# Performance work log

Measured on AMD Instinct MI355X. Metric: run time of the kernel, lower is better.

The kernel has to match this reference:

```python
import jax, jax.numpy as jnp
import numpy as np

D_HEAD = 64


def precompute_rope(d_head, max_seq_len):
    theta = 10000.0 ** (-jnp.arange(0, d_head, 2, dtype=jnp.float32) / d_head)
    positions = jnp.arange(max_seq_len, dtype=jnp.float32)
    angles = jnp.outer(positions, theta)  # [T, d_head/2]
    cos = jnp.repeat(jnp.cos(angles), 2, axis=-1)  # [T, d_head]
    sin = jnp.repeat(jnp.sin(angles), 2, axis=-1)
    return cos, sin


def apply_rope(x, cos, sin):
    # x: [B, H, T, d_head]; cos/sin: [T, d_head] (already sliced to T)
    x_even = x[..., 0::2]
    x_odd = x[..., 1::2]
    x2 = jnp.stack([-x_odd, x_even], axis=-1).reshape(x.shape)  # rotate-half interleaved
    return x * cos + x2 * sin


def setup_inputs() -> dict:
    key = jax.random.key(0)
    k1, k2, k3 = jax.random.split(key, 3)
    B, T, C = 4, 2048, 1024
    x = jax.random.normal(k1, (B, T, C), dtype=jnp.float32)
    mask = jnp.tril(jnp.ones((T, T), dtype=jnp.int32))[None, None]  # causal [1,1,T,T]
    Wqkv = jax.random.normal(k2, (3 * C, C), dtype=jnp.float32) * (1.0 / np.sqrt(C))
    Wout = jax.random.normal(k3, (C, C), dtype=jnp.float32) * (1.0 / np.sqrt(C))
    return {"x": x, "mask": mask, "Wqkv": Wqkv, "Wout": Wout}


def reference(x, mask, Wqkv, Wout):
    B, T, C = x.shape
    n_heads = 16
    d_head = C // n_heads
    cos, sin = precompute_rope(d_head, T)

    qkv = (x @ Wqkv.T).reshape(B, T, 3, n_heads, d_head)
    q, k, v = qkv[:, :, 0], qkv[:, :, 1], qkv[:, :, 2]
    q = jnp.transpose(q, (0, 2, 1, 3))  # [B, H, T, d]
    k = jnp.transpose(k, (0, 2, 1, 3))
    v = jnp.transpose(v, (0, 2, 1, 3))

    q = apply_rope(q, cos, sin)
    k = apply_rope(k, cos, sin)

    attn = jnp.einsum('bhqd,bhkd->bhqk', q, k) / jnp.sqrt(jnp.float32(d_head))
    attn = jnp.where(mask[:, :, :T, :T] == 0, -jnp.inf, attn)
    attn = jax.nn.softmax(attn, axis=-1)

    out = jnp.einsum('bhqk,bhkd->bhqd', attn, v)
    out = jnp.transpose(out, (0, 2, 1, 3)).reshape(B, T, C)
    return out @ Wout.T
```

## Files before the change

kernel.cpp:

```cpp
#include <hip/hip_runtime.h>

typedef unsigned short u16;
typedef unsigned int   u32;
typedef __bf16 bf16;
typedef bf16  bf16x8 __attribute__((ext_vector_type(8)));
typedef u16   u16x8  __attribute__((ext_vector_type(8)));
typedef u32   u32x4  __attribute__((ext_vector_type(4)));
typedef float f32x4  __attribute__((ext_vector_type(4)));
typedef float f32x16 __attribute__((ext_vector_type(16)));

__device__ __forceinline__ u16 f2bf(float f) {
  u32 u = __builtin_bit_cast(u32, f);
  u32 r = u + 0x7fffu + ((u >> 16) & 1u);
  return (u16)(r >> 16);
}

__device__ __forceinline__ u32 cvtpk(float lo, float hi) {
  u32 r;
  asm("v_cvt_pk_bf16_f32 %0, %1, %2" : "=v"(r) : "v"(lo), "v"(hi));
  return r;
}

__device__ __forceinline__ bf16x8 ldb8(const u16* p) {
  return __builtin_bit_cast(bf16x8, *reinterpret_cast<const u16x8*>(p));
}

__device__ __forceinline__ f32x4 mfma16(bf16x8 a, bf16x8 b, f32x4 c) {
  return __builtin_amdgcn_mfma_f32_16x16x32_bf16(a, b, c, 0, 0, 0);
}

__device__ __forceinline__ f32x16 mfma32(bf16x8 a, bf16x8 b, f32x16 c) {
  return __builtin_amdgcn_mfma_f32_32x32x16_bf16(a, b, c, 0, 0, 0);
}

__device__ __forceinline__ void gl_lds16(const void* g, void* l) {
  __builtin_amdgcn_global_load_lds(
      (const __attribute__((address_space(1))) void*)g,
      (__attribute__((address_space(3))) void*)l, 16, 0, 0);
}

__device__ __forceinline__ void stage128x64(const u16* gbase, u16* lds, int tid) {
#pragma unroll
  for (int rd = 0; rd < 4; rd++) {
    int o = rd * 4096 + tid * 16;
    int row = o >> 7, colb = o & 127;
    gl_lds16((const char*)gbase + (size_t)row * 2048 + colb, (char*)lds + o);
  }
}

__device__ __forceinline__ size_t qk_frag_addr(int bh, int t, int d) {
  return (size_t)bh * 131072 + (size_t)(t >> 5) * 2048 +
         (size_t)((d >> 4) * 512 + ((d >> 3) & 1) * 256 + (t & 31) * 8 + (d & 7));
}
__device__ __forceinline__ size_t v_frag_addr(int bh, int t, int d) {
  return (size_t)bh * 131072 + (size_t)(t >> 5) * 2048 +
         (size_t)((d >> 5) * 1024 + ((t >> 4) & 1) * 512 +
                  (((t >> 3) & 1) * 32 + (d & 31)) * 8 + (t & 7));
}

__global__ void cvt_bf16(const float* __restrict__ in, u16* __restrict__ out, int n4) {
  int stride = gridDim.x * blockDim.x;
  for (int i = blockIdx.x * blockDim.x + threadIdx.x; i < n4; i += stride) {
    float4 f = reinterpret_cast<const float4*>(in)[i];
    ushort4 o;
    o.x = f2bf(f.x); o.y = f2bf(f.y); o.z = f2bf(f.z); o.w = f2bf(f.w);
    reinterpret_cast<ushort4*>(out)[i] = o;
  }
}

__global__ void rope_tab(float* __restrict__ ct, float* __restrict__ st) {
  int idx = blockIdx.x * 256 + threadIdx.x;
  int t = idx >> 5, i = idx & 31;
  float theta = exp2f(-(float)i * 0.4152410118609203f);
  float ang = (float)t * theta;
  ct[idx] = cosf(ang);
  st[idx] = sinf(ang);
}

__global__ __launch_bounds__(256) void gemm_qkv(
    const u16* __restrict__ xb, const u16* __restrict__ wb,
    u16* __restrict__ qfb, u16* __restrict__ kfb, u16* __restrict__ vfb,
    const float* __restrict__ cost, const float* __restrict__ sint) {
  __shared__ u16 As[128 * 64];
  __shared__ u16 Bs[128 * 64];
  int tid = threadIdx.x, lane = tid & 63, w = tid >> 6;
  int wm = w >> 1, wn = w & 1;
  int lr = lane & 15, lk = lane >> 4;
  int m0 = blockIdx.y * 128, n0 = blockIdx.x * 128;

  f32x4 acc[4][4] = {};

  for (int k0 = 0; k0 < 1024; k0 += 64) {
    stage128x64(xb + (size_t)m0 * 1024 + k0, As, tid);
    stage128x64(wb + (size_t)n0 * 1024 + k0, Bs, tid);
    asm volatile("s_waitcnt vmcnt(0)" ::: "memory");
    __syncthreads();
#pragma unroll
    for (int kk = 0; kk < 2; kk++) {
      bf16x8 af[4], bfr[4];
#pragma unroll
      for (int mt = 0; mt < 4; mt++) af[mt]  = ldb8(&As[(64 * wm + 16 * mt + lr) * 64 + lk * 8 + 32 * kk]);
#pragma unroll
      for (int nt = 0; nt < 4; nt++) bfr[nt] = ldb8(&Bs[(64 * wn + 16 * nt + lr) * 64 + lk * 8 + 32 * kk]);
#pragma unroll
      for (int mt = 0; mt < 4; mt++)
#pragma unroll
        for (int nt = 0; nt < 4; nt++)
          acc[mt][nt] = mfma16(af[mt], bfr[nt], acc[mt][nt]);
    }
    __syncthreads();
  }

  const float CQ = 0.18033688011112042f;
#pragma unroll
  for (int nt = 0; nt < 4; nt++) {
    int col = n0 + 64 * wn + 16 * nt + lr;
    int sec = col >> 10;
    int cc = col & 1023;
    int h = cc >> 6, d = cc & 63;
    if (sec < 2) {
      u16* buf = (sec == 0) ? qfb : kfb;
      float scale = (sec == 0) ? CQ : 1.0f;
#pragma unroll
      for (int mt = 0; mt < 4; mt++) {
        int Mb = m0 + 64 * wm + 16 * mt + lk * 4;
#pragma unroll
        for (int r = 0; r < 4; r++) {
          int M = Mb + r;
          int b = M >> 11, t = M & 2047;
          float val = acc[mt][nt][r];
          float par = __shfl_xor(val, 1);
          float c_ = cost[t * 32 + (d >> 1)];
          float s_ = sint[t * 32 + (d >> 1)];
          float res = (d & 1) ? (val * c_ + par * s_) : (val * c_ - par * s_);
          buf[qk_frag_addr(b * 16 + h, t, d)] = f2bf(res * scale);
        }
      }
    } else {
#pragma unroll
      for (int mt = 0; mt < 4; mt++) {
        int Mb = m0 + 64 * wm + 16 * mt + lk * 4;
        int b = Mb >> 11, t = Mb & 2047;
        ushort4 pk;
        pk.x = f2bf(acc[mt][nt][0]); pk.y = f2bf(acc[mt][nt][1]);
        pk.z = f2bf(acc[mt][nt][2]); pk.w = f2bf(acc[mt][nt][3]);
        *reinterpret_cast<ushort4*>(&vfb[v_frag_addr(b * 16 + h, t, d)]) = pk;
      }
    }
  }
}


__device__ __forceinline__ void attn_step(
    const u16* __restrict__ kfb, const u16* __restrict__ vfb,
    const bf16x8* qf, int kt, int qt, int qrow,
    int lane, int hi,
    f32x16& o0, f32x16& o1, float& m_, float& l_) {
  const u16* ktb = kfb + (size_t)kt * 2048;
  const u16* vtb = vfb + (size_t)kt * 2048;
  bf16x8 vf00 = ldb8(vtb + lane * 8);
  bf16x8 vf01 = ldb8(vtb + 512 + lane * 8);
  bf16x8 vf10 = ldb8(vtb + 1024 + lane * 8);
  bf16x8 vf11 = ldb8(vtb + 1536 + lane * 8);

  f32x16 sT = {};
#pragma unroll
  for (int s = 0; s < 4; s++) {
    bf16x8 kf = ldb8(ktb + s * 512 + lane * 8);
    sT = mfma32(kf, qf[s], sT);
  }
  if (kt == qt) {
    int k0 = kt * 32;
#pragma unroll
    for (int r = 0; r < 16; r++) {
      int kvg = k0 + (r & 3) + 8 * (r >> 2) + 4 * hi;
      if (kvg > qrow) sT[r] = -3.0e38f;
    }
  }
  float a0 = fmaxf(fmaxf(sT[0], sT[1]),  fmaxf(sT[2], sT[3]));
  float a1 = fmaxf(fmaxf(sT[4], sT[5]),  fmaxf(sT[6], sT[7]));
  float a2 = fmaxf(fmaxf(sT[8], sT[9]),  fmaxf(sT[10], sT[11]));
  float a3 = fmaxf(fmaxf(sT[12], sT[13]), fmaxf(sT[14], sT[15]));
  float pm = fmaxf(fmaxf(a0, a1), fmaxf(a2, a3));
  pm = fmaxf(pm, __shfl_xor(pm, 32));

  if (__any(pm > m_ + 8.0f)) {
    float mn = fmaxf(m_, pm);
    float corr = exp2f(m_ - mn);
    l_ *= corr;
    o0 *= corr; o1 *= corr;
    m_ = mn;
  }

  float p[16];
#pragma unroll
  for (int r = 0; r < 16; r++) p[r] = exp2f(sT[r] - m_);
  float r0 = (p[0] + p[1]) + (p[2] + p[3]);
  float r1 = (p[4] + p[5]) + (p[6] + p[7]);
  float r2 = (p[8] + p[9]) + (p[10] + p[11]);
  float r3 = (p[12] + p[13]) + (p[14] + p[15]);
  float rs = (r0 + r1) + (r2 + r3);
  rs += __shfl_xor(rs, 32);
  l_ += rs;

  u32 c0 = cvtpk(p[0], p[1]),   c1 = cvtpk(p[2], p[3]);
  u32 c2 = cvtpk(p[4], p[5]),   c3 = cvtpk(p[6], p[7]);
  u32 c4 = cvtpk(p[8], p[9]),   c5 = cvtpk(p[10], p[11]);
  u32 c6 = cvtpk(p[12], p[13]), c7 = cvtpk(p[14], p[15]);
  u32 x0 = __shfl_xor((int)c0, 32), x1 = __shfl_xor((int)c1, 32);
  u32 x2 = __shfl_xor((int)c2, 32), x3 = __shfl_xor((int)c3, 32);
  u32 x4 = __shfl_xor((int)c4, 32), x5 = __shfl_xor((int)c5, 32);
  u32 x6 = __shfl_xor((int)c6, 32), x7 = __shfl_xor((int)c7, 32);
  u32x4 w0 = { hi ? x2 : c0, hi ? x3 : c1, hi ? c2 : x0, hi ? c3 : x1 };
  u32x4 w1 = { hi ? x6 : c4, hi ? x7 : c5, hi ? c6 : x4, hi ? c7 : x5 };
  bf16x8 pf0 = __builtin_bit_cast(bf16x8, w0);
  bf16x8 pf1 = __builtin_bit_cast(bf16x8, w1);

  o0 = mfma32(vf00, pf0, o0);
  o0 = mfma32(vf01, pf1, o0);
  o1 = mfma32(vf10, pf0, o1);
  o1 = mfma32(vf11, pf1, o1);
}

__device__ __forceinline__ void stash_state(
    float* o_l, float* ml, int lane,
    const f32x16& o0, const f32x16& o1, float m_, float l_) {
#pragma unroll
  for (int r = 0; r < 16; r++) {
    o_l[r * 64 + lane]        = o0[r];
    o_l[(16 + r) * 64 + lane] = o1[r];
  }
  ml[lane]      = m_;
  ml[64 + lane] = l_;
}

__device__ __forceinline__ void merge_state(
    const float* o_l, const float* ml, int lane,
    f32x16& o0, f32x16& o1, float& m_, float& l_) {
  float me = ml[lane], le = ml[64 + lane];
  float mn = fmaxf(m_, me);
  float sc = exp2f(m_ - mn), se = exp2f(me - mn);
  l_ = l_ * sc + le * se;
#pragma unroll
  for (int r = 0; r < 16; r++) {
    o0[r] = o0[r] * sc + o_l[r * 64 + lane] * se;
    o1[r] = o1[r] * sc + o_l[(16 + r) * 64 + lane] * se;
  }
  m_ = mn;
}

__device__ __forceinline__ void attn_half(
    const u16* __restrict__ qfb, const u16* __restrict__ kfb,
    const u16* __restrict__ vfb, u16* __restrict__ og,
    float* o_lds, float* ml_lds,
    int qt, int kt0, int w, int lane, int l31, int hi,
    size_t outbase) {
  int qrow = qt * 32 + l31;
  bf16x8 qf[4];
#pragma unroll
  for (int s = 0; s < 4; s++)
    qf[s] = ldb8(qfb + (size_t)qt * 2048 + s * 512 + lane * 8);

  f32x16 o0 = {}, o1 = {};
  float m_ = -3.0e38f, l_ = 0.f;

#pragma unroll 1
  for (int kt = kt0; kt <= qt; kt += 4)
    attn_step(kfb, vfb, qf, kt, qt, qrow, lane, hi, o0, o1, m_, l_);

  if (w >= 2) stash_state(o_lds + (w - 2) * 2048, ml_lds + (w - 2) * 128, lane, o0, o1, m_, l_);
  __syncthreads();
  if (w < 2)  merge_state(o_lds + w * 2048, ml_lds + w * 128, lane, o0, o1, m_, l_);
  __syncthreads();
  if (w == 1) stash_state(o_lds, ml_lds, lane, o0, o1, m_, l_);
  __syncthreads();
  if (w == 0) {
    merge_state(o_lds, ml_lds, lane, o0, o1, m_, l_);
    float inv = 1.0f / l_;
    size_t base = outbase + (size_t)qrow * 1024;
#pragma unroll
    for (int db = 0; db < 2; db++) {
      f32x16 oo = db ? o1 : o0;
#pragma unroll
      for (int r = 0; r < 16; r += 2) {
        int d = db * 32 + (r & 3) + 8 * (r >> 2) + 4 * hi;
        u32 pk_ = cvtpk(oo[r] * inv, oo[r + 1] * inv);
        *reinterpret_cast<u32*>(&og[base + d]) = pk_;
      }
    }
  }
  __syncthreads();
}

__global__ __launch_bounds__(256, 4) void attn_fwd(
    const u16* __restrict__ qg, const u16* __restrict__ kg,
    const u16* __restrict__ vg, u16* __restrict__ og) {
  __shared__ float o_lds[2 * 32 * 64];
  __shared__ float ml_lds[2 * 2 * 64];
  int tid = threadIdx.x, lane = tid & 63, w = tid >> 6;
  int l31 = lane & 31, hi = lane >> 5;
  int blk = blockIdx.x;
  int bh = blk & 63, i = blk >> 6;
  const u16* qfb = qg + (size_t)bh * 131072;
  const u16* kfb = kg + (size_t)bh * 131072;
  const u16* vfb = vg + (size_t)bh * 131072;
  int hh = bh & 15, b = bh >> 4;
  size_t outbase = (size_t)b * 2048 * 1024 + hh * 64;

  attn_half(qfb, kfb, vfb, og, o_lds, ml_lds, i, w, w, lane, l31, hi, outbase);
  attn_half(qfb, kfb, vfb, og, o_lds, ml_lds, 63 - i, (w - i - 1) & 3, w, lane, l31, hi, outbase);
}

__global__ __launch_bounds__(256) void gemm_out(
    const u16* __restrict__ ab, const u16* __restrict__ wb, float* __restrict__ out) {
  __shared__ u16 As[128 * 64];
  __shared__ u16 Bs[128 * 64];
  int tid = threadIdx.x, lane = tid & 63, w = tid >> 6;
  int wm = w >> 1, wn = w & 1;
  int lr = lane & 15, lk = lane >> 4;
  int m0 = blockIdx.y * 128, n0 = blockIdx.x * 128;

  f32x4 acc[4][4] = {};

  for (int k0 = 0; k0 < 1024; k0 += 64) {
    stage128x64(ab + (size_t)m0 * 1024 + k0, As, tid);
    stage128x64(wb + (size_t)n0 * 1024 + k0, Bs, tid);
    asm volatile("s_waitcnt vmcnt(0)" ::: "memory");
    __syncthreads();
#pragma unroll
    for (int kk = 0; kk < 2; kk++) {
      bf16x8 af[4], bfr[4];
#pragma unroll
      for (int mt = 0; mt < 4; mt++) af[mt]  = ldb8(&As[(64 * wm + 16 * mt + lr) * 64 + lk * 8 + 32 * kk]);
#pragma unroll
      for (int nt = 0; nt < 4; nt++) bfr[nt] = ldb8(&Bs[(64 * wn + 16 * nt + lr) * 64 + lk * 8 + 32 * kk]);
#pragma unroll
      for (int mt = 0; mt < 4; mt++)
#pragma unroll
        for (int nt = 0; nt < 4; nt++)
          acc[mt][nt] = mfma16(af[mt], bfr[nt], acc[mt][nt]);
    }
    __syncthreads();
  }

#pragma unroll
  for (int nt = 0; nt < 4; nt++) {
    int col = n0 + 64 * wn + 16 * nt + lr;
#pragma unroll
    for (int mt = 0; mt < 4; mt++) {
      int Mb = m0 + 64 * wm + 16 * mt + lk * 4;
#pragma unroll
      for (int r = 0; r < 4; r++) {
        out[(size_t)(Mb + r) * 1024 + col] = acc[mt][nt][r];
      }
    }
  }
}

extern "C" void kernel_launch(void* const* d_in, const int* in_sizes, int n_in,
                              void* d_out, int out_size, void* d_ws, size_t ws_size,
                              hipStream_t stream) {
  const float* x    = (const float*)d_in[0];
  const float* Wqkv = (const float*)d_in[2];
  const float* Wout = (const float*)d_in[3];
  float* out = (float*)d_out;
  char* ws = (char*)d_ws;

  u16* x_bf    = (u16*)(ws + 0);
  u16* wqkv_bf = (u16*)(ws + 16777216);
  u16* wout_bf = (u16*)(ws + 23068672);
  u16* qf_buf  = (u16*)(ws + 25165824);
  u16* kf_buf  = (u16*)(ws + 41943040);
  u16* vf_buf  = (u16*)(ws + 58720256);
  u16* a_out   = (u16*)(ws + 75497472);
  float* cost  = (float*)(ws + 92274688);
  float* sint  = (float*)(ws + 92536832);

  cvt_bf16<<<2048, 256, 0, stream>>>(x, x_bf, 8388608 / 4);
  cvt_bf16<<<768, 256, 0, stream>>>(Wqkv, wqkv_bf, 3145728 / 4);
  cvt_bf16<<<256, 256, 0, stream>>>(Wout, wout_bf, 1048576 / 4);
  rope_tab<<<256, 256, 0, stream>>>(cost, sint);
  gemm_qkv<<<dim3(24, 64), 256, 0, stream>>>(x_bf, wqkv_bf, qf_buf, kf_buf, vf_buf, cost, sint);
  attn_fwd<<<2048, 256, 0, stream>>>(qf_buf, kf_buf, vf_buf, a_out);
  gemm_out<<<dim3(8, 64), 256, 0, stream>>>(a_out, wout_bf, out);
}
```

Measured before the change: 204.8 us.

## Stage QK RoPE epilogue through LDS with fragment-ordered tables and shrink out-GEMM tile

The QKV GEMM epilogue for Q and K now writes accumulators to LDS, then each thread reads 8 contiguous values and applies RoPE. It uses cos/sin tables precomputed in the fragment layout and writes 16-byte packed bf16 stores instead of scattered 2-byte stores with shuffles. The rope table doubles in size and the epilogue adds LDS round-trips and barriers. The output GEMM tile narrows from 128 to 64 columns to double the block count (512 to 1024), trading per-block reuse for better CU occupancy.

```diff
diff --git a/kernel.cpp b/kernel.cpp
--- a/kernel.cpp
+++ b/kernel.cpp
@@ -48,6 +48,15 @@
   }
 }
 
+__device__ __forceinline__ void stage64x64(const u16* gbase, u16* lds, int tid) {
+#pragma unroll
+  for (int rd = 0; rd < 2; rd++) {
+    int o = rd * 4096 + tid * 16;
+    int row = o >> 7, colb = o & 127;
+    gl_lds16((const char*)gbase + (size_t)row * 2048 + colb, (char*)lds + o);
+  }
+}
+
 __device__ __forceinline__ size_t qk_frag_addr(int bh, int t, int d) {
   return (size_t)bh * 131072 + (size_t)(t >> 5) * 2048 +
          (size_t)((d >> 4) * 512 + ((d >> 3) & 1) * 256 + (t & 31) * 8 + (d & 7));
@@ -68,10 +77,13 @@
   }
 }
 
-__global__ void rope_tab(float* __restrict__ ct, float* __restrict__ st) {
+__global__ void rope_tab_frag(float* __restrict__ ct, float* __restrict__ st) {
   int idx = blockIdx.x * 256 + threadIdx.x;
-  int t = idx >> 5, i = idx & 31;
-  float theta = exp2f(-(float)i * 0.4152410118609203f);
+  int tile = idx >> 11, off = idx & 2047;
+  int s = off >> 9, h = (off >> 8) & 1, t5 = (off >> 3) & 31, j = off & 7;
+  int t = tile * 32 + t5;
+  int d = s * 16 + h * 8 + j;
+  float theta = exp2f(-(float)(d >> 1) * 0.4152410118609203f);
   float ang = (float)t * theta;
   ct[idx] = cosf(ang);
   st[idx] = sinf(ang);
@@ -80,9 +92,10 @@
 __global__ __launch_bounds__(256) void gemm_qkv(
     const u16* __restrict__ xb, const u16* __restrict__ wb,
     u16* __restrict__ qfb, u16* __restrict__ kfb, u16* __restrict__ vfb,
-    const float* __restrict__ cost, const float* __restrict__ sint) {
-  __shared__ u16 As[128 * 64];
-  __shared__ u16 Bs[128 * 64];
+    const float* __restrict__ ctf, const float* __restrict__ stf) {
+  __shared__ u16 sb[2][128 * 64];
+  u16* As = sb[0];
+  u16* Bs = sb[1];
   int tid = threadIdx.x, lane = tid & 63, w = tid >> 6;
   int wm = w >> 1, wn = w & 1;
   int lr = lane & 15, lk = lane >> 4;
@@ -112,31 +125,55 @@
   }
 
   const float CQ = 0.18033688011112042f;
-#pragma unroll
-  for (int nt = 0; nt < 4; nt++) {
-    int col = n0 + 64 * wn + 16 * nt + lr;
-    int sec = col >> 10;
-    int cc = col & 1023;
-    int h = cc >> 6, d = cc & 63;
-    if (sec < 2) {
-      u16* buf = (sec == 0) ? qfb : kfb;
-      float scale = (sec == 0) ? CQ : 1.0f;
-#pragma unroll
-      for (int mt = 0; mt < 4; mt++) {
-        int Mb = m0 + 64 * wm + 16 * mt + lk * 4;
-#pragma unroll
-        for (int r = 0; r < 4; r++) {
-          int M = Mb + r;
-          int b = M >> 11, t = M & 2047;
-          float val = acc[mt][nt][r];
-          float par = __shfl_xor(val, 1);
-          float c_ = cost[t * 32 + (d >> 1)];
-          float s_ = sint[t * 32 + (d >> 1)];
-          float res = (d & 1) ? (val * c_ + par * s_) : (val * c_ - par * s_);
-          buf[qk_frag_addr(b * 16 + h, t, d)] = f2bf(res * scale);
-        }
+  int sec = n0 >> 10;
+
+  if (sec < 2) {
+    u16* dstbuf = (sec == 0) ? qfb : kfb;
+    float scale = (sec == 0) ? CQ : 1.0f;
+    float* ep = (float*)sb;
+#pragma unroll
+    for (int nt = 0; nt < 4; nt++) {
+      __syncthreads();
+#pragma unroll
+      for (int mt = 0; mt < 4; mt++)
+#pragma unroll
+        for (int r = 0; r < 4; r++)
+          ep[(64 * wm + 16 * mt + lk * 4 + r) * 36 + wn * 16 + lr] = acc[mt][nt][r];
+      __syncthreads();
+#pragma unroll
+      for (int i = 0; i < 2; i++) {
+        int chunk = tid + 256 * i;
+        int h = chunk & 1, strip = (chunk >> 1) & 1, row = chunk >> 2;
+        const float* src = &ep[row * 36 + strip * 16 + h * 8];
+        float v0 = src[0], v1 = src[1], v2 = src[2], v3 = src[3];
+        float v4 = src[4], v5 = src[5], v6 = src[6], v7 = src[7];
+        int M = m0 + row;
+        int b = M >> 11, tt = M & 2047;
+        int gcol = n0 + strip * 64 + nt * 16 + h * 8;
+        int hh = (gcol & 1023) >> 6;
+        size_t tix = (size_t)(tt >> 5) * 2048 + nt * 512 + h * 256 + (tt & 31) * 8;
+        float4 c0 = *reinterpret_cast<const float4*>(&ctf[tix]);
+        float4 c1 = *reinterpret_cast<const float4*>(&ctf[tix + 4]);
+        float4 s0 = *reinterpret_cast<const float4*>(&stf[tix]);
+        float4 s1 = *reinterpret_cast<const float4*>(&stf[tix + 4]);
+        float e0 = (v0 * c0.x - v1 * s0.x) * scale;
+        float e1 = (v1 * c0.y + v0 * s0.y) * scale;
+        float e2 = (v2 * c0.z - v3 * s0.z) * scale;
+        float e3 = (v3 * c0.w + v2 * s0.w) * scale;
+        float e4 = (v4 * c1.x - v5 * s1.x) * scale;
+        float e5 = (v5 * c1.y + v4 * s1.y) * scale;
+        float e6 = (v6 * c1.z - v7 * s1.z) * scale;
+        float e7 = (v7 * c1.w + v6 * s1.w) * scale;
+        u32x4 pk = { cvtpk(e0, e1), cvtpk(e2, e3), cvtpk(e4, e5), cvtpk(e6, e7) };
+        *reinterpret_cast<u32x4*>(&dstbuf[(size_t)(b * 16 + hh) * 131072 + tix]) = pk;
       }
-    } else {
+    }
+  } else {
+#pragma unroll
+    for (int nt = 0; nt < 4; nt++) {
+      int col = n0 + 64 * wn + 16 * nt + lr;
+      int cc = col & 1023;
+      int h = cc >> 6, d = cc & 63;
 #pragma unroll
       for (int mt = 0; mt < 4; mt++) {
         int Mb = m0 + 64 * wm + 16 * mt + lk * 4;
@@ -149,7 +186,6 @@
     }
   }
 }
-
 
 __device__ __forceinline__ void attn_step(
     const u16* __restrict__ kfb, const u16* __restrict__ vfb,
@@ -314,38 +350,38 @@
 __global__ __launch_bounds__(256) void gemm_out(
     const u16* __restrict__ ab, const u16* __restrict__ wb, float* __restrict__ out) {
   __shared__ u16 As[128 * 64];
-  __shared__ u16 Bs[128 * 64];
+  __shared__ u16 Bs[64 * 64];
   int tid = threadIdx.x, lane = tid & 63, w = tid >> 6;
   int wm = w >> 1, wn = w & 1;
   int lr = lane & 15, lk = lane >> 4;
-  int m0 = blockIdx.y * 128, n0 = blockIdx.x * 128;
-
-  f32x4 acc[4][4] = {};
+  int m0 = blockIdx.y * 128, n0 = blockIdx.x * 64;
+
+  f32x4 acc[4][2] = {};
 
   for (int k0 = 0; k0 < 1024; k0 += 64) {
     stage128x64(ab + (size_t)m0 * 1024 + k0, As, tid);
-    stage128x64(wb + (size_t)n0 * 1024 + k0, Bs, tid);
+    stage64x64(wb + (size_t)n0 * 1024 + k0, Bs, tid);
     asm volatile("s_waitcnt vmcnt(0)" ::: "memory");
     __syncthreads();
 #pragma unroll
     for (int kk = 0; kk < 2; kk++) {
-      bf16x8 af[4], bfr[4];
+      bf16x8 af[4], bfr[2];
 #pragma unroll
       for (int mt = 0; mt < 4; mt++) af[mt]  = ldb8(&As[(64 * wm + 16 * mt + lr) * 64 + lk * 8 + 32 * kk]);
 #pragma unroll
-      for (int nt = 0; nt < 4; nt++) bfr[nt] = ldb8(&Bs[(64 * wn + 16 * nt + lr) * 64 + lk * 8 + 32 * kk]);
+      for (int nt = 0; nt < 2; nt++) bfr[nt] = ldb8(&Bs[(32 * wn + 16 * nt + lr) * 64 + lk * 8 + 32 * kk]);
 #pragma unroll
       for (int mt = 0; mt < 4; mt++)
 #pragma unroll
-        for (int nt = 0; nt < 4; nt++)
+        for (int nt = 0; nt < 2; nt++)
           acc[mt][nt] = mfma16(af[mt], bfr[nt], acc[mt][nt]);
     }
     __syncthreads();
   }
 
 #pragma unroll
-  for (int nt = 0; nt < 4; nt++) {
-    int col = n0 + 64 * wn + 16 * nt + lr;
+  for (int nt = 0; nt < 2; nt++) {
+    int col = n0 + 32 * wn + 16 * nt + lr;
 #pragma unroll
     for (int mt = 0; mt < 4; mt++) {
       int Mb = m0 + 64 * wm + 16 * mt + lk * 4;
@@ -373,14 +409,14 @@
   u16* kf_buf  = (u16*)(ws + 41943040);
   u16* vf_buf  = (u16*)(ws + 58720256);
   u16* a_out   = (u16*)(ws + 75497472);
-  float* cost  = (float*)(ws + 92274688);
-  float* sint  = (float*)(ws + 92536832);
+  float* ctf   = (float*)(ws + 92274688);
+  float* stf   = (float*)(ws + 92798976);
 
   cvt_bf16<<<2048, 256, 0, stream>>>(x, x_bf, 8388608 / 4);
   cvt_bf16<<<768, 256, 0, stream>>>(Wqkv, wqkv_bf, 3145728 / 4);
   cvt_bf16<<<256, 256, 0, stream>>>(Wout, wout_bf, 1048576 / 4);
-  rope_tab<<<256, 256, 0, stream>>>(cost, sint);
-  gemm_qkv<<<dim3(24, 64), 256, 0, stream>>>(x_bf, wqkv_bf, qf_buf, kf_buf, vf_buf, cost, sint);
+  rope_tab_frag<<<512, 256, 0, stream>>>(ctf, stf);
+  gemm_qkv<<<dim3(24, 64), 256, 0, stream>>>(x_bf, wqkv_bf, qf_buf, kf_buf, vf_buf, ctf, stf);
   attn_fwd<<<2048, 256, 0, stream>>>(qf_buf, kf_buf, vf_buf, a_out);
-  gemm_out<<<dim3(8, 64), 256, 0, stream>>>(a_out, wout_bf, out);
-}
+  gemm_out<<<dim3(16, 64), 256, 0, stream>>>(a_out, wout_bf, out);
+}
```

Measured after the change: 206.6 us. Within noise of the previous version (+0.9%).

## Double-buffer QKV GEMM with swizzled LDS, bigger tiles, and narrower out-proj tiles

Applied to the files above, without the earlier changes.

The QKV projection GEMM moves to a 256x128 tile with 512 threads and double-buffered LDS. Global-to-LDS loads for the next K step are issued while MFMAs run on the current buffer, and an XOR swizzle on the LDS layout is meant to cut bank conflicts. MFMA sections are wrapped in s_setprio. The output projection GEMM narrows its N tile to 64 so the grid has twice as many blocks, trading some per-block reuse for better CU occupancy.

```diff
diff --git a/kernel.cpp b/kernel.cpp
--- a/kernel.cpp
+++ b/kernel.cpp
@@ -47,6 +47,21 @@
     gl_lds16((const char*)gbase + (size_t)row * 2048 + colb, (char*)lds + o);
   }
 }
+__device__ __forceinline__ void stage64x64(const u16* gbase, u16* lds, int tid) {
+#pragma unroll
+  for (int rd = 0; rd < 2; rd++) {
+    int o = rd * 4096 + tid * 16;
+    int row = o >> 7, colb = o & 127;
+    gl_lds16((const char*)gbase + (size_t)row * 2048 + colb, (char*)lds + o);
+  }
+}
+
+__device__ __forceinline__ void stage_swz(const u16* g, u16* lds, int tid, int rd) {
+  int o = rd * 8192 + tid * 16;
+  int row = o >> 7;
+  int slot = (tid & 7) ^ (row & 7);
+  gl_lds16((const char*)g + (size_t)row * 2048 + slot * 16, (char*)lds + o);
+}
 
 __device__ __forceinline__ size_t qk_frag_addr(int bh, int t, int d) {
   return (size_t)bh * 131072 + (size_t)(t >> 5) * 2048 +
@@ -77,79 +92,127 @@
   st[idx] = sinf(ang);
 }
 
-__global__ __launch_bounds__(256) void gemm_qkv(
+__global__ __launch_bounds__(512) void gemm_qkv(
     const u16* __restrict__ xb, const u16* __restrict__ wb,
     u16* __restrict__ qfb, u16* __restrict__ kfb, u16* __restrict__ vfb,
     const float* __restrict__ cost, const float* __restrict__ sint) {
-  __shared__ u16 As[128 * 64];
-  __shared__ u16 Bs[128 * 64];
-  int tid = threadIdx.x, lane = tid & 63, w = tid >> 6;
-  int wm = w >> 1, wn = w & 1;
+  __shared__ u16 As[2][256 * 64];
+  __shared__ u16 Bs[2][128 * 64];
+  int tid = threadIdx.x, lane = tid & 63, wid = tid >> 6;
+  int wm = wid >> 1, wn = wid & 1;
   int lr = lane & 15, lk = lane >> 4;
-  int m0 = blockIdx.y * 128, n0 = blockIdx.x * 128;
+  int m0 = blockIdx.y * 256, n0 = blockIdx.x * 128;
+  const u16* gA = xb + (size_t)m0 * 1024;
+  const u16* gB = wb + (size_t)n0 * 1024;
+  int swz = lr & 7;
 
   f32x4 acc[4][4] = {};
 
-  for (int k0 = 0; k0 < 1024; k0 += 64) {
-    stage128x64(xb + (size_t)m0 * 1024 + k0, As, tid);
-    stage128x64(wb + (size_t)n0 * 1024 + k0, Bs, tid);
+#pragma unroll
+  for (int rd = 0; rd < 4; rd++) stage_swz(gA, As[0], tid, rd);
+#pragma unroll
+  for (int rd = 0; rd < 2; rd++) stage_swz(gB, Bs[0], tid, rd);
+  asm volatile("s_waitcnt vmcnt(0)" ::: "memory");
+  __syncthreads();
+
+#pragma unroll 1
+  for (int t = 0; t < 16; t++) {
+    int cur = t & 1;
+    const u16* Ac = As[cur];
+    const u16* Bc = Bs[cur];
+    u16* An = As[cur ^ 1];
+    u16* Bn = Bs[cur ^ 1];
+    const u16* gAn = gA + (t + 1) * 64;
+    const u16* gBn = gB + (t + 1) * 64;
+    bf16x8 af[4], bfr[4];
+
+#pragma unroll
+    for (int mr = 0; mr < 4; mr++)
+      af[mr] = ldb8(&Ac[(wm * 64 + mr * 16 + lr) * 64 + ((lk ^ swz) * 8)]);
+#pragma unroll
+    for (int nr = 0; nr < 4; nr++)
+      bfr[nr] = ldb8(&Bc[(wn * 64 + nr * 16 + lr) * 64 + ((lk ^ swz) * 8)]);
+    if (t < 15) {
+      stage_swz(gAn, An, tid, 0);
+      stage_swz(gAn, An, tid, 1);
+      stage_swz(gBn, Bn, tid, 0);
+    }
+    __builtin_amdgcn_s_setprio(1);
+#pragma unroll
+    for (int mr = 0; mr < 4; mr++)
+#pragma unroll
+      for (int nr = 0; nr < 4; nr++)
+        acc[mr][nr] = mfma16(af[mr], bfr[nr], acc[mr][nr]);
+    __builtin_amdgcn_s_setprio(0);
+    __builtin_amdgcn_s_barrier();
+
+#pragma unroll
+    for (int mr = 0; mr < 4; mr++)
+      af[mr] = ldb8(&Ac[(wm * 64 + mr * 16 + lr) * 64 + (((lk + 4) ^ swz) * 8)]);
+#pragma unroll
+    for (int nr = 0; nr < 4; nr++)
+      bfr[nr] = ldb8(&Bc[(wn * 64 + nr * 16 + lr) * 64 + (((lk + 4) ^ swz) * 8)]);
+    if (t < 15) {
+      stage_swz(gAn, An, tid, 2);
+      stage_swz(gAn, An, tid, 3);
+      stage_swz(gBn, Bn, tid, 1);
+    }
+    __builtin_amdgcn_s_setprio(1);
+#pragma unroll
+    for (int mr = 0; mr < 4; mr++)
+#pragma unroll
+      for (int nr = 0; nr < 4; nr++)
+        acc[mr][nr] = mfma16(af[mr], bfr[nr], acc[mr][nr]);
+    __builtin_amdgcn_s_setprio(0);
     asm volatile("s_waitcnt vmcnt(0)" ::: "memory");
-    __syncthreads();
-#pragma unroll
-    for (int kk = 0; kk < 2; kk++) {
-      bf16x8 af[4], bfr[4];
-#pragma unroll
-      for (int mt = 0; mt < 4; mt++) af[mt]  = ldb8(&As[(64 * wm + 16 * mt + lr) * 64 + lk * 8 + 32 * kk]);
-#pragma unroll
-      for (int nt = 0; nt < 4; nt++) bfr[nt] = ldb8(&Bs[(64 * wn + 16 * nt + lr) * 64 + lk * 8 + 32 * kk]);
-#pragma unroll
-      for (int mt = 0; mt < 4; mt++)
-#pragma unroll
-        for (int nt = 0; nt < 4; nt++)
-          acc[mt][nt] = mfma16(af[mt], bfr[nt], acc[mt][nt]);
-    }
-    __syncthreads();
+    __builtin_amdgcn_s_barrier();
   }
 
   const float CQ = 0.18033688011112042f;
-#pragma unroll
-  for (int nt = 0; nt < 4; nt++) {
-    int col = n0 + 64 * wn + 16 * nt + lr;
-    int sec = col >> 10;
-    int cc = col & 1023;
-    int h = cc >> 6, d = cc & 63;
-    if (sec < 2) {
-      u16* buf = (sec == 0) ? qfb : kfb;
-      float scale = (sec == 0) ? CQ : 1.0f;
-#pragma unroll
-      for (int mt = 0; mt < 4; mt++) {
-        int Mb = m0 + 64 * wm + 16 * mt + lk * 4;
+  int sec = n0 >> 10;
+
+  if (sec < 2) {
+    u16* buf = (sec == 0) ? qfb : kfb;
+    float scale = (sec == 0) ? CQ : 1.0f;
+#pragma unroll
+    for (int nr = 0; nr < 4; nr++) {
+      int col = n0 + wn * 64 + nr * 16 + lr;
+      int cc = col & 1023;
+      int h = cc >> 6, d = cc & 63;
+#pragma unroll
+      for (int mr = 0; mr < 4; mr++) {
+        int Mb = m0 + wm * 64 + mr * 16 + lk * 4;
 #pragma unroll
         for (int r = 0; r < 4; r++) {
           int M = Mb + r;
-          int b = M >> 11, t = M & 2047;
-          float val = acc[mt][nt][r];
+          int b = M >> 11, tt = M & 2047;
+          float val = acc[mr][nr][r];
           float par = __shfl_xor(val, 1);
-          float c_ = cost[t * 32 + (d >> 1)];
-          float s_ = sint[t * 32 + (d >> 1)];
+          float c_ = cost[tt * 32 + (d >> 1)];
+          float s_ = sint[tt * 32 + (d >> 1)];
           float res = (d & 1) ? (val * c_ + par * s_) : (val * c_ - par * s_);
-          buf[qk_frag_addr(b * 16 + h, t, d)] = f2bf(res * scale);
+          buf[qk_frag_addr(b * 16 + h, tt, d)] = f2bf(res * scale);
         }
       }
-    } else {
-#pragma unroll
-      for (int mt = 0; mt < 4; mt++) {
-        int Mb = m0 + 64 * wm + 16 * mt + lk * 4;
-        int b = Mb >> 11, t = Mb & 2047;
+    }
+  } else {
+#pragma unroll
+    for (int nr = 0; nr < 4; nr++) {
+      int col = n0 + wn * 64 + nr * 16 + lr;
+      int cc = col & 1023;
+      int h = cc >> 6, d = cc & 63;
+#pragma unroll
+      for (int mr = 0; mr < 4; mr++) {
+        int Mb = m0 + wm * 64 + mr * 16 + lk * 4;
+        int b = Mb >> 11, tt = Mb & 2047;
         ushort4 pk;
-        pk.x = f2bf(acc[mt][nt][0]); pk.y = f2bf(acc[mt][nt][1]);
-        pk.z = f2bf(acc[mt][nt][2]); pk.w = f2bf(acc[mt][nt][3]);
-        *reinterpret_cast<ushort4*>(&vfb[v_frag_addr(b * 16 + h, t, d)]) = pk;
+        pk.x = f2bf(acc[mr][nr][0]); pk.y = f2bf(acc[mr][nr][1]);
+        pk.z = f2bf(acc[mr][nr][2]); pk.w = f2bf(acc[mr][nr][3]);
+        *reinterpret_cast<ushort4*>(&vfb[v_frag_addr(b * 16 + h, tt, d)]) = pk;
       }
     }
   }
 }
-
 
 __device__ __forceinline__ void attn_step(
     const u16* __restrict__ kfb, const u16* __restrict__ vfb,
@@ -314,38 +377,38 @@
 __global__ __launch_bounds__(256) void gemm_out(
     const u16* __restrict__ ab, const u16* __restrict__ wb, float* __restrict__ out) {
   __shared__ u16 As[128 * 64];
-  __shared__ u16 Bs[128 * 64];
+  __shared__ u16 Bs[64 * 64];
   int tid = threadIdx.x, lane = tid & 63, w = tid >> 6;
   int wm = w >> 1, wn = w & 1;
   int lr = lane & 15, lk = lane >> 4;
-  int m0 = blockIdx.y * 128, n0 = blockIdx.x * 128;
-
-  f32x4 acc[4][4] = {};
+  int m0 = blockIdx.y * 128, n0 = blockIdx.x * 64;
+
+  f32x4 acc[4][2] = {};
 
   for (int k0 = 0; k0 < 1024; k0 += 64) {
     stage128x64(ab + (size_t)m0 * 1024 + k0, As, tid);
-    stage128x64(wb + (size_t)n0 * 1024 + k0, Bs, tid);
+    stage64x64(wb + (size_t)n0 * 1024 + k0, Bs, tid);
     asm volatile("s_waitcnt vmcnt(0)" ::: "memory");
     __syncthreads();
 #pragma unroll
     for (int kk = 0; kk < 2; kk++) {
-      bf16x8 af[4], bfr[4];
+      bf16x8 af[4], bfr[2];
 #pragma unroll
       for (int mt = 0; mt < 4; mt++) af[mt]  = ldb8(&As[(64 * wm + 16 * mt + lr) * 64 + lk * 8 + 32 * kk]);
 #pragma unroll
-      for (int nt = 0; nt < 4; nt++) bfr[nt] = ldb8(&Bs[(64 * wn + 16 * nt + lr) * 64 + lk * 8 + 32 * kk]);
+      for (int nt = 0; nt < 2; nt++) bfr[nt] = ldb8(&Bs[(32 * wn + 16 * nt + lr) * 64 + lk * 8 + 32 * kk]);
 #pragma unroll
       for (int mt = 0; mt < 4; mt++)
 #pragma unroll
-        for (int nt = 0; nt < 4; nt++)
+        for (int nt = 0; nt < 2; nt++)
           acc[mt][nt] = mfma16(af[mt], bfr[nt], acc[mt][nt]);
     }
     __syncthreads();
   }
 
 #pragma unroll
-  for (int nt = 0; nt < 4; nt++) {
-    int col = n0 + 64 * wn + 16 * nt + lr;
+  for (int nt = 0; nt < 2; nt++) {
+    int col = n0 + 32 * wn + 16 * nt + lr;
 #pragma unroll
     for (int mt = 0; mt < 4; mt++) {
       int Mb = m0 + 64 * wm + 16 * mt + lk * 4;
@@ -380,7 +443,7 @@
   cvt_bf16<<<768, 256, 0, stream>>>(Wqkv, wqkv_bf, 3145728 / 4);
   cvt_bf16<<<256, 256, 0, stream>>>(Wout, wout_bf, 1048576 / 4);
   rope_tab<<<256, 256, 0, stream>>>(cost, sint);
-  gemm_qkv<<<dim3(24, 64), 256, 0, stream>>>(x_bf, wqkv_bf, qf_buf, kf_buf, vf_buf, cost, sint);
+  gemm_qkv<<<dim3(24, 32), 512, 0, stream>>>(x_bf, wqkv_bf, qf_buf, kf_buf, vf_buf, cost, sint);
   attn_fwd<<<2048, 256, 0, stream>>>(qf_buf, kf_buf, vf_buf, a_out);
-  gemm_out<<<dim3(8, 64), 256, 0, stream>>>(a_out, wout_bf, out);
-}
+  gemm_out<<<dim3(16, 64), 256, 0, stream>>>(a_out, wout_bf, out);
+}
```

New measurement: 188.6 us. 7.9% less time.
